# Optimization experiments

Measured on AMD Instinct MI355X. Metric: run time of the kernel, lower is better.

The kernel has to match this reference:

```python
import jax, jax.numpy as jnp
import numpy as np

D_MODEL = 768
D_STATE = 64
HEADDIM = 64
CHUNK = 64
EXPAND = 2
D_CONV = 4
D_INNER = EXPAND * D_MODEL          # 1536
NHEADS = D_INNER // HEADDIM         # 24
CONV_CH = D_INNER + 2 * D_STATE     # 1664
D_IN_PROJ = 2 * D_INNER + 2 * D_STATE + NHEADS  # 3224
EPS = 1e-5


def segsum(x):
    # x: (..., T) -> (..., T, T); entry [i, j] = sum_{k=j+1..i} x[k] for i>=j, -inf above diag
    T = x.shape[-1]
    cs = jnp.cumsum(x, axis=-1)
    seg = cs[..., :, None] - cs[..., None, :]
    mask = jnp.tril(jnp.ones((T, T), dtype=bool))
    return jnp.where(mask, seg, -jnp.inf)


def ssd(x, A, B, C, chunk):
    # x: (b, L, h, p), A: (b, L, h), B/C: (b, L, n)
    b, L, h, p = x.shape
    nc = L // chunk
    x = x.reshape(b, nc, chunk, h, p)
    A = A.reshape(b, nc, chunk, h).transpose(0, 3, 1, 2)   # (b, h, nc, l)
    B = B.reshape(b, nc, chunk, -1)
    C = C.reshape(b, nc, chunk, -1)
    A_cs = jnp.cumsum(A, axis=-1)                          # (b, h, nc, l)
    Lm = jnp.exp(segsum(A))                                # (b, h, nc, l, s)
    # intra-chunk (diagonal) term
    Y_diag = jnp.einsum('bcln,bcsn,bhcls,bcshp->bclhp', C, B, Lm, x)
    # per-chunk states
    decay_states = jnp.exp(A_cs[..., -1:] - A_cs)          # (b, h, nc, l)
    states = jnp.einsum('bcln,bhcl,bclhp->bchpn', B, decay_states, x)
    states = jnp.concatenate([jnp.zeros_like(states[:, :1]), states], axis=1)
    # inter-chunk recurrence via segsum over chunk totals
    chunk_sums = jnp.pad(A_cs[..., -1], ((0, 0), (0, 0), (1, 0)))
    decay_chunk = jnp.exp(segsum(chunk_sums))              # (b, h, nc+1, nc+1)
    new_states = jnp.einsum('bhzc,bchpn->bzhpn', decay_chunk, states)
    states = new_states[:, :-1]                            # (b, nc, h, p, n)
    Y_off = jnp.einsum('bcln,bchpn,bhcl->bclhp', C, states, jnp.exp(A_cs))
    return (Y_diag + Y_off).reshape(b, L, h, p)


def setup_inputs() -> dict:
    key = jax.random.key(0)
    ks = jax.random.split(key, 6)
    b, L = 2, 4096
    u = jax.random.normal(ks[0], (b, L, D_MODEL), dtype=jnp.float32)
    W_in = jax.random.normal(ks[1], (D_IN_PROJ, D_MODEL), dtype=jnp.float32) * (D_MODEL ** -0.5)
    conv_w = jax.random.normal(ks[2], (CONV_CH, 1, D_CONV), dtype=jnp.float32) * 0.3
    conv_b = jnp.zeros((CONV_CH,), dtype=jnp.float32)
    dt_bias = jnp.zeros((NHEADS,), dtype=jnp.float32)
    A_log = jax.random.normal(ks[3], (NHEADS,), dtype=jnp.float32) * 0.1
    D = jnp.ones((NHEADS,), dtype=jnp.float32)
    norm_w = jnp.ones((D_INNER,), dtype=jnp.float32)
    W_out = jax.random.normal(ks[4], (D_MODEL, D_INNER), dtype=jnp.float32) * (D_INNER ** -0.5)
    return {'u': u, 'W_in': W_in, 'conv_w': conv_w, 'conv_b': conv_b,
            'dt_bias': dt_bias, 'A_log': A_log, 'D': D, 'norm_w': norm_w, 'W_out': W_out}


def reference(u, W_in, conv_w, conv_b, dt_bias, A_log, D, norm_w, W_out):
    b, L, _ = u.shape
    zxbcdt = u @ W_in.T                                    # (b, L, d_in_proj)
    z = zxbcdt[..., :D_INNER]
    xBC = zxbcdt[..., D_INNER:D_INNER + CONV_CH]
    dt = jax.nn.softplus(zxbcdt[..., -NHEADS:] + dt_bias)  # (b, L, h)
    # causal depthwise conv (left pad d_conv-1, matches torch pad+slice)
    xBC = jax.lax.conv_general_dilated(
        xBC.transpose(0, 2, 1), conv_w, (1,), [(D_CONV - 1, 0)],
        dimension_numbers=('NCH', 'OIH', 'NCH'), feature_group_count=CONV_CH)
    xBC = jax.nn.silu(xBC.transpose(0, 2, 1) + conv_b)
    x = xBC[..., :D_INNER].reshape(b, L, NHEADS, HEADDIM)
    Bm = xBC[..., D_INNER:D_INNER + D_STATE]
    Cm = xBC[..., -D_STATE:]
    A = -jnp.exp(A_log)                                    # (h,)
    y = ssd(x * dt[..., None], A * dt, Bm, Cm, CHUNK)
    y = y + x * D[None, None, :, None]
    y = y.reshape(b, L, D_INNER)
    # gated RMSNorm
    y = y * jax.nn.silu(z)
    y = y * jax.lax.rsqrt(jnp.mean(y * y, axis=-1, keepdims=True) + EPS) * norm_w
    return y @ W_out.T
```

## Files before the change

### kernel.cpp

```cpp
#include <hip/hip_runtime.h>

typedef __attribute__((ext_vector_type(4))) float f4;
typedef __attribute__((ext_vector_type(8))) short bfx8;
typedef __attribute__((ext_vector_type(4))) float f32x4;
typedef __attribute__((ext_vector_type(4))) unsigned int u32x4;
typedef __attribute__((ext_vector_type(4))) unsigned short u16x4;
typedef __attribute__((ext_vector_type(8))) unsigned short u16x8;
typedef unsigned short ushort_t;

#define DM 768
#define DINNER 1536
#define NH 24
#define XBCW 1664
#define DINPROJ 3224
#define NPAD1 3328
#define NCHUNK 64
#define BROWS 8192
#define PADB 72

__device__ inline ushort_t f2bf(float f) {
    unsigned u = __builtin_bit_cast(unsigned, f);
    unsigned r = (u + 0x7FFF + ((u >> 16) & 1)) >> 16;
    return (ushort_t)r;
}
__device__ inline float bf2f(ushort_t u) {
    return __builtin_bit_cast(float, (unsigned)u << 16);
}
__device__ inline void gl16(const void* g, void* l) {
    __builtin_amdgcn_global_load_lds((const __attribute__((address_space(1))) void*)g,
                                     (__attribute__((address_space(3))) void*)l, 16, 0, 0);
}

__global__ __launch_bounds__(256) void fill_kernel(float* out, int n, float v) {
    int i = blockIdx.x * 256 + threadIdx.x;
    if (i < n) out[i] = v;
}

__global__ __launch_bounds__(256) void cvt_kernel(const float* __restrict__ in,
                                                  ushort_t* __restrict__ outp, long n4) {
    long i = (long)blockIdx.x * 256 + threadIdx.x;
    if (i >= n4) return;
    f4 v = *(const f4*)&in[i * 4];
    u16x4 o;
    o[0] = f2bf(v[0]); o[1] = f2bf(v[1]); o[2] = f2bf(v[2]); o[3] = f2bf(v[3]);
    *(u16x4*)&outp[i * 4] = o;
}

__global__ __launch_bounds__(256) void cvt_pad_kernel(const float* __restrict__ in,
                                                      ushort_t* __restrict__ outp) {
    long q = (long)blockIdx.x * 256 + threadIdx.x;
    if (q >= (long)NPAD1 * 192) return;
    int row = (int)(q / 192);
    int cq = (int)(q % 192);
    u16x4 o = {0, 0, 0, 0};
    if (row < DINPROJ) {
        f4 v = *(const f4*)&in[(long)row * DM + cq * 4];
        o[0] = f2bf(v[0]); o[1] = f2bf(v[1]); o[2] = f2bf(v[2]); o[3] = f2bf(v[3]);
    }
    *(u16x4*)&outp[q * 4] = o;
}

template <int EPI>
__global__ __launch_bounds__(256) void gemm_bt(const ushort_t* __restrict__ A,
                                               const ushort_t* __restrict__ B,
                                               float* __restrict__ C,
                                               int K, int ldc,
                                               ushort_t* __restrict__ zbf,
                                               float* __restrict__ xbcraw,
                                               float* __restrict__ dtbT,
                                               const float* __restrict__ dt_bias) {
    __shared__ __align__(16) ushort_t As[2][128 * 32];
    __shared__ __align__(16) ushort_t Bs[2][128 * 32];
    int tid = threadIdx.x;
    int lane = tid & 63;
    int w = tid >> 6;
    int wr = w >> 1, wc = w & 1;
    int m0 = blockIdx.y * 128;
    int n0 = blockIdx.x * 128;
    int r16 = lane & 15, kg = lane >> 4;

    int row0 = tid >> 2, cof0 = (tid & 3) * 8;
    const ushort_t* a0 = &A[(long)(m0 + row0) * K + cof0];
    const ushort_t* a1 = &A[(long)(m0 + row0 + 64) * K + cof0];
    const ushort_t* b0 = &B[(long)(n0 + row0) * K + cof0];
    const ushort_t* b1 = &B[(long)(n0 + row0 + 64) * K + cof0];
    char* asb[2] = {(char*)&As[0][0] + w * 1024, (char*)&As[1][0] + w * 1024};
    char* bsb[2] = {(char*)&Bs[0][0] + w * 1024, (char*)&Bs[1][0] + w * 1024};

    f32x4 acc[4][4] = {};

    gl16(a0, asb[0]); gl16(a1, asb[0] + 4096);
    gl16(b0, bsb[0]); gl16(b1, bsb[0] + 4096);
    asm volatile("s_waitcnt vmcnt(0)" ::: "memory");
    __builtin_amdgcn_s_barrier();

    int nk = K >> 5;
    for (int t = 0; t < nk; ++t) {
        int cur = t & 1;
        if (t + 1 < nk) {
            int k1 = (t + 1) << 5;
            gl16(a0 + k1, asb[cur ^ 1]); gl16(a1 + k1, asb[cur ^ 1] + 4096);
            gl16(b0 + k1, bsb[cur ^ 1]); gl16(b1 + k1, bsb[cur ^ 1] + 4096);
        }
        const ushort_t* Asc = &As[cur][0];
        const ushort_t* Bsc = &Bs[cur][0];
        bfx8 af[4], bfr[4];
#pragma unroll
        for (int i = 0; i < 4; ++i) {
            af[i] = *(const bfx8*)&Asc[(wr * 64 + i * 16 + r16) * 32 + kg * 8];
            bfr[i] = *(const bfx8*)&Bsc[(wc * 64 + i * 16 + r16) * 32 + kg * 8];
        }
#pragma unroll
        for (int i = 0; i < 4; ++i)
#pragma unroll
            for (int j = 0; j < 4; ++j)
                acc[i][j] = __builtin_amdgcn_mfma_f32_16x16x32_bf16(af[i], bfr[j], acc[i][j], 0, 0, 0);
        asm volatile("s_waitcnt vmcnt(0) lgkmcnt(0)" ::: "memory");
        __builtin_amdgcn_sched_barrier(0);
        __builtin_amdgcn_s_barrier();
    }

#pragma unroll
    for (int i = 0; i < 4; ++i) {
        int rowb = m0 + wr * 64 + i * 16 + kg * 4;
#pragma unroll
        for (int j = 0; j < 4; ++j) {
            int col = n0 + wc * 64 + j * 16 + r16;
            if (EPI == 0) {
#pragma unroll
                for (int q = 0; q < 4; ++q)
                    C[(long)(rowb + q) * ldc + col] = acc[i][j][q];
            } else {
                if (n0 < DINNER) {
#pragma unroll
                    for (int q = 0; q < 4; ++q)
                        zbf[(long)(rowb + q) * DINNER + col] = f2bf(acc[i][j][q]);
                } else if (n0 < 3200) {
#pragma unroll
                    for (int q = 0; q < 4; ++q)
                        xbcraw[(long)(rowb + q) * XBCW + col - DINNER] = acc[i][j][q];
                } else if (col < DINPROJ) {
                    int h = col - 3200;
                    float bias = dt_bias[h];
#pragma unroll
                    for (int q = 0; q < 4; ++q) {
                        float v = acc[i][j][q] + bias;
                        float d = (v > 20.f) ? v : log1pf(__expf(v));
                        dtbT[(long)h * BROWS + rowb + q] = d;
                    }
                }
            }
        }
    }
}

__global__ __launch_bounds__(256) void conv_kernel(const float* __restrict__ xin,
                                                   const float* __restrict__ cw,
                                                   const float* __restrict__ cb,
                                                   ushort_t* __restrict__ xbc) {
    int ch = blockIdx.y * 256 + threadIdx.x;
    int row = blockIdx.x;
    if (ch >= XBCW) return;
    int b = row >> 12;
    int l = row & 4095;
    float acc = cb[ch];
#pragma unroll
    for (int k = 0; k < 4; ++k) {
        int ll = l - 3 + k;
        if (ll >= 0)
            acc += cw[ch * 4 + k] * xin[(long)(b * 4096 + ll) * XBCW + ch];
    }
    float s = acc / (1.f + __expf(-acc));
    xbc[(long)row * XBCW + ch] = f2bf(s);
}

__global__ __launch_bounds__(256) void acs_kernel(const float* __restrict__ dtbT,
                                                  const float* __restrict__ A_log,
                                                  float* __restrict__ acs,
                                                  float* __restrict__ Tsum) {
    int bh = blockIdx.x;
    int b = bh / NH, h = bh % NH;
    int t = threadIdx.x;
    int lane = t & 63;
    float A = -__expf(A_log[h]);
    const float* dp = &dtbT[(long)h * BROWS + b * 4096];
#pragma unroll
    for (int it = 0; it < 16; ++it) {
        int c = (t >> 6) + 4 * it;
        float v = A * dp[c * 64 + lane];
#pragma unroll
        for (int off = 1; off < 64; off <<= 1) {
            float u = __shfl_up(v, off, 64);
            if (lane >= off) v += u;
        }
        acs[((long)bh * NCHUNK + c) * 64 + lane] = v;
        if (lane == 63) Tsum[bh * NCHUNK + c] = v;
    }
}

__global__ __launch_bounds__(256) void states_kernel(const ushort_t* __restrict__ xbc,
                                                     const float* __restrict__ dtbT,
                                                     const float* __restrict__ acs,
                                                     const float* __restrict__ Tsum,
                                                     ushort_t* __restrict__ states) {
    int h = blockIdx.x, c = blockIdx.y, b = blockIdx.z;
    __shared__ __align__(16) ushort_t Wt[64 * PADB];
    __shared__ __align__(16) ushort_t Bt[64 * PADB];
    int t = threadIdx.x;
    long rowg0 = (long)b * 4096 + c * 64;
    long acsb = ((long)(b * NH + h) * NCHUNK + c) * 64;
    float T = Tsum[(b * NH + h) * NCHUNK + c];
#pragma unroll
    for (int i = 0; i < 2; ++i) {
        int q = t + 256 * i;
        int l = q >> 3, sg = q & 7;
        const ushort_t* rp = &xbc[(rowg0 + l) * (long)XBCW];
        float dec = dtbT[(long)h * BROWS + rowg0 + l] * __expf(T - acs[acsb + l]);
        u16x8 xv = *(const u16x8*)&rp[h * 64 + sg * 8];
        u16x8 bv = *(const u16x8*)&rp[DINNER + sg * 8];
#pragma unroll
        for (int jj = 0; jj < 8; ++jj) {
            Wt[(sg * 8 + jj) * PADB + l] = f2bf(bf2f(xv[jj]) * dec);
            Bt[(sg * 8 + jj) * PADB + l] = bv[jj];
        }
    }
    __syncthreads();
    int w = t >> 6, lane = t & 63;
    int r16 = lane & 15, kg = lane >> 4;
    bfx8 aw[2];
#pragma unroll
    for (int kk = 0; kk < 2; ++kk)
        aw[kk] = *(const bfx8*)&Wt[(w * 16 + r16) * PADB + kk * 32 + kg * 8];
    f32x4 acc[4] = {};
#pragma unroll
    for (int j = 0; j < 4; ++j)
#pragma unroll
        for (int kk = 0; kk < 2; ++kk) {
            bfx8 bb = *(const bfx8*)&Bt[(j * 16 + r16) * PADB + kk * 32 + kg * 8];
            acc[j] = __builtin_amdgcn_mfma_f32_16x16x32_bf16(aw[kk], bb, acc[j], 0, 0, 0);
        }
    __syncthreads();
#pragma unroll
    for (int j = 0; j < 4; ++j)
#pragma unroll
        for (int q = 0; q < 4; ++q)
            Wt[(w * 16 + kg * 4 + q) * PADB + j * 16 + r16] = f2bf(acc[j][q]);
    __syncthreads();
    long ob = ((long)(b * NH + h) * NCHUNK + c) * 4096;
#pragma unroll
    for (int i = 0; i < 2; ++i) {
        int q = t + 256 * i;
        int p = q >> 3, sg = q & 7;
        *(u16x8*)&states[ob + p * 64 + sg * 8] = *(const u16x8*)&Wt[p * PADB + sg * 8];
    }
}

__global__ __launch_bounds__(256) void scan_kernel(const float* __restrict__ Tsum,
                                                   ushort_t* __restrict__ states) {
    int e = blockIdx.x * 256 + threadIdx.x;
    int h = blockIdx.y, b = blockIdx.z;
    long base = ((long)(b * NH + h)) * NCHUNK * 4096 + e;
    const float* Tp = &Tsum[(b * NH + h) * NCHUNK];
    float acc = 0.f;
    for (int c = 0; c < NCHUNK; ++c) {
        float cur = bf2f(states[base + (long)c * 4096]);
        states[base + (long)c * 4096] = f2bf(acc);
        acc = __expf(Tp[c]) * acc + cur;
    }
}

__global__ __launch_bounds__(256) void yfull_kernel(const ushort_t* __restrict__ xbc,
                                                    const float* __restrict__ dtbT,
                                                    const float* __restrict__ acs,
                                                    const ushort_t* __restrict__ sprev,
                                                    ushort_t* __restrict__ ybuf) {
    int h = blockIdx.x, c = blockIdx.y, b = blockIdx.z;
    __shared__ __align__(16) ushort_t Cb[64 * PADB];
    __shared__ __align__(16) ushort_t Bb[64 * PADB];
    __shared__ __align__(16) ushort_t Xt[64 * PADB];
    __shared__ __align__(16) ushort_t Sp[64 * PADB];
    __shared__ __align__(16) ushort_t Sm[64 * PADB];
    __shared__ float sAcs[64], sE[64];
    int t = threadIdx.x;
    long rowg0 = (long)b * 4096 + c * 64;
    long acsb = ((long)(b * NH + h) * NCHUNK + c) * 64;
    long spb = ((long)(b * NH + h) * NCHUNK + c) * 4096;
    if (t < 64) {
        float a = acs[acsb + t];
        sAcs[t] = a;
        sE[t] = __expf(a);
    }
#pragma unroll
    for (int i = 0; i < 2; ++i) {
        int q = t + 256 * i;
        int l = q >> 3, sg = q & 7;
        const ushort_t* rp = &xbc[(rowg0 + l) * (long)XBCW];
        *(u16x8*)&Cb[l * PADB + sg * 8] = *(const u16x8*)&rp[1600 + sg * 8];
        *(u16x8*)&Bb[l * PADB + sg * 8] = *(const u16x8*)&rp[DINNER + sg * 8];
        float dtv = dtbT[(long)h * BROWS + rowg0 + l];
        u16x8 xv = *(const u16x8*)&rp[h * 64 + sg * 8];
#pragma unroll
        for (int jj = 0; jj < 8; ++jj)
            Xt[(sg * 8 + jj) * PADB + l] = f2bf(bf2f(xv[jj]) * dtv);
        *(u16x8*)&Sp[l * PADB + sg * 8] = *(const u16x8*)&sprev[spb + l * 64 + sg * 8];
    }
    __syncthreads();
    int w = t >> 6, lane = t & 63;
    int r16 = lane & 15, kg = lane >> 4;
    bfx8 ac[2];
#pragma unroll
    for (int kk = 0; kk < 2; ++kk)
        ac[kk] = *(const bfx8*)&Cb[(w * 16 + r16) * PADB + kk * 32 + kg * 8];
    f32x4 s_acc[4] = {};
#pragma unroll
    for (int j = 0; j < 4; ++j)
#pragma unroll
        for (int kk = 0; kk < 2; ++kk) {
            bfx8 bb = *(const bfx8*)&Bb[(j * 16 + r16) * PADB + kk * 32 + kg * 8];
            s_acc[j] = __builtin_amdgcn_mfma_f32_16x16x32_bf16(ac[kk], bb, s_acc[j], 0, 0, 0);
        }
#pragma unroll
    for (int j = 0; j < 4; ++j)
#pragma unroll
        for (int q = 0; q < 4; ++q) {
            int l = w * 16 + kg * 4 + q;
            int s = j * 16 + r16;
            float v = s_acc[j][q];
            v = (s <= l) ? v * __expf(sAcs[l] - sAcs[s]) : 0.f;
            Sm[l * PADB + s] = f2bf(v);
        }
    __syncthreads();
    bfx8 as[2];
#pragma unroll
    for (int kk = 0; kk < 2; ++kk)
        as[kk] = *(const bfx8*)&Sm[(w * 16 + r16) * PADB + kk * 32 + kg * 8];
    f32x4 d_acc[4] = {}, o_acc[4] = {};
#pragma unroll
    for (int j = 0; j < 4; ++j)
#pragma unroll
        for (int kk = 0; kk < 2; ++kk) {
            bfx8 xb = *(const bfx8*)&Xt[(j * 16 + r16) * PADB + kk * 32 + kg * 8];
            d_acc[j] = __builtin_amdgcn_mfma_f32_16x16x32_bf16(as[kk], xb, d_acc[j], 0, 0, 0);
            bfx8 sb = *(const bfx8*)&Sp[(j * 16 + r16) * PADB + kk * 32 + kg * 8];
            o_acc[j] = __builtin_amdgcn_mfma_f32_16x16x32_bf16(ac[kk], sb, o_acc[j], 0, 0, 0);
        }
#pragma unroll
    for (int j = 0; j < 4; ++j)
#pragma unroll
        for (int q = 0; q < 4; ++q) {
            int l = w * 16 + kg * 4 + q;
            int p = j * 16 + r16;
            Bb[l * PADB + p] = f2bf(d_acc[j][q] + sE[l] * o_acc[j][q]);
        }
    __syncthreads();
#pragma unroll
    for (int i = 0; i < 2; ++i) {
        int q = t + 256 * i;
        int l = q >> 3, sg = q & 7;
        *(u16x8*)&ybuf[(rowg0 + l) * (long)DINNER + h * 64 + sg * 8] =
            *(const u16x8*)&Bb[l * PADB + sg * 8];
    }
}

__global__ __launch_bounds__(256) void norm_kernel(const ushort_t* __restrict__ ybuf,
                                                   const ushort_t* __restrict__ xbc,
                                                   const ushort_t* __restrict__ zbf,
                                                   const float* __restrict__ Dp,
                                                   const float* __restrict__ normw,
                                                   ushort_t* __restrict__ ybf) {
    int row = blockIdx.x;
    int t = threadIdx.x;
    float g[6];
    float ss = 0.f;
#pragma unroll
    for (int i = 0; i < 6; ++i) {
        int j = t + 256 * i;
        int h = j >> 6;
        float x = bf2f(xbc[(long)row * XBCW + j]);
        float yy = bf2f(ybuf[(long)row * DINNER + j]) + x * Dp[h];
        float z = bf2f(zbf[(long)row * DINNER + j]);
        float gz = z / (1.f + __expf(-z));
        float v = yy * gz;
        g[i] = v;
        ss += v * v;
    }
#pragma unroll
    for (int o = 32; o > 0; o >>= 1) ss += __shfl_xor(ss, o, 64);
    __shared__ float wsum[4];
    __shared__ float sscale;
    int w = t >> 6;
    if ((t & 63) == 0) wsum[w] = ss;
    __syncthreads();
    if (t == 0) {
        float tot = wsum[0] + wsum[1] + wsum[2] + wsum[3];
        sscale = rsqrtf(tot / (float)DINNER + 1e-5f);
    }
    __syncthreads();
    float sc = sscale;
#pragma unroll
    for (int i = 0; i < 6; ++i) {
        int j = t + 256 * i;
        ybf[(long)row * DINNER + j] = f2bf(g[i] * sc * normw[j]);
    }
}

extern "C" void kernel_launch(void* const* d_in, const int* in_sizes, int n_in,
                              void* d_out, int out_size, void* d_ws, size_t ws_size,
                              hipStream_t stream) {
    const float* u = (const float*)d_in[0];
    const float* W_in = (const float*)d_in[1];
    const float* conv_w = (const float*)d_in[2];
    const float* conv_b = (const float*)d_in[3];
    const float* dt_bias = (const float*)d_in[4];
    const float* A_log = (const float*)d_in[5];
    const float* Dp = (const float*)d_in[6];
    const float* norm_w = (const float*)d_in[7];
    const float* W_out = (const float*)d_in[8];
    float* out = (float*)d_out;

    char* ws = (char*)d_ws;
    size_t off = 0;
    auto alloc = [&](size_t bytes) {
        void* p = ws + off;
        off += (bytes + 255) & ~(size_t)255;
        return p;
    };
    ushort_t* zbf = (ushort_t*)alloc((size_t)BROWS * DINNER * 2);
    float* xbcraw = (float*)alloc((size_t)BROWS * XBCW * 4);
    ushort_t* xbc = (ushort_t*)alloc((size_t)BROWS * XBCW * 2);
    float* dtbT = (float*)alloc((size_t)NH * BROWS * 4);
    float* acs = (float*)alloc((size_t)2 * NH * NCHUNK * 64 * 4);
    float* Tsum = (float*)alloc((size_t)2 * NH * NCHUNK * 4);
    ushort_t* states = (ushort_t*)alloc((size_t)2 * NH * NCHUNK * 4096 * 2);
    ushort_t* ybuf = (ushort_t*)alloc((size_t)BROWS * DINNER * 2);
    ushort_t* ybf = (ushort_t*)xbcraw;
    ushort_t* ubf = ybuf;
    ushort_t* winbf = states;
    ushort_t* woutbf = states;

    if (off > ws_size) {
        fill_kernel<<<(out_size + 255) / 256, 256, 0, stream>>>(out, out_size, 12345.0f);
        return;
    }

    cvt_kernel<<<(BROWS * DM / 4 + 255) / 256, 256, 0, stream>>>(u, ubf, (long)BROWS * DM / 4);
    cvt_pad_kernel<<<((long)NPAD1 * 192 + 255) / 256, 256, 0, stream>>>(W_in, winbf);

    gemm_bt<1><<<dim3(26, 64), 256, 0, stream>>>(ubf, winbf, nullptr, DM, 0,
                                                 zbf, xbcraw, dtbT, dt_bias);

    conv_kernel<<<dim3(BROWS, 7), 256, 0, stream>>>(xbcraw, conv_w, conv_b, xbc);

    acs_kernel<<<2 * NH, 256, 0, stream>>>(dtbT, A_log, acs, Tsum);
    states_kernel<<<dim3(NH, NCHUNK, 2), 256, 0, stream>>>(xbc, dtbT, acs, Tsum, states);
    scan_kernel<<<dim3(16, NH, 2), 256, 0, stream>>>(Tsum, states);
    yfull_kernel<<<dim3(NH, NCHUNK, 2), 256, 0, stream>>>(xbc, dtbT, acs, states, ybuf);

    norm_kernel<<<BROWS, 256, 0, stream>>>(ybuf, xbc, zbf, Dp, norm_w, ybf);

    cvt_kernel<<<(DM * DINNER / 4 + 255) / 256, 256, 0, stream>>>(W_out, woutbf, (long)DM * DINNER / 4);
    gemm_bt<0><<<dim3(6, 64), 256, 0, stream>>>(ybf, woutbf, out, DINNER, DM,
                                                nullptr, nullptr, nullptr, nullptr);
}
```

Before: 280.2 us.

## Triple-buffer GEMM LDS pipeline and store pre-conv xBC as bf16

The shared bf16 GEMM moves from a double-buffered LDS loop to a three-stage ring. Tiles are prefetched two iterations ahead, and each iteration waits with a partial vmcnt and a single barrier before compute, so global loads overlap more MFMA work. Separately, the raw xBC projection output is written as bf16 instead of fp32, halving the bytes written by the in-projection and read by the conv kernel. This adds LDS usage (48KB per block), which may lower occupancy, and rounds the pre-convolution values to bf16.

Result: no change. 278.7 us (-0.5%).

```diff
diff --git a/kernel.cpp b/kernel.cpp
--- a/kernel.cpp
+++ b/kernel.cpp
@@ -66,11 +66,11 @@
                                                float* __restrict__ C,
                                                int K, int ldc,
                                                ushort_t* __restrict__ zbf,
-                                               float* __restrict__ xbcraw,
+                                               ushort_t* __restrict__ xbcbf,
                                                float* __restrict__ dtbT,
                                                const float* __restrict__ dt_bias) {
-    __shared__ __align__(16) ushort_t As[2][128 * 32];
-    __shared__ __align__(16) ushort_t Bs[2][128 * 32];
+    __shared__ __align__(16) ushort_t As[3][128 * 32];
+    __shared__ __align__(16) ushort_t Bs[3][128 * 32];
     int tid = threadIdx.x;
     int lane = tid & 63;
     int w = tid >> 6;
@@ -84,26 +84,34 @@
     const ushort_t* a1 = &A[(long)(m0 + row0 + 64) * K + cof0];
     const ushort_t* b0 = &B[(long)(n0 + row0) * K + cof0];
     const ushort_t* b1 = &B[(long)(n0 + row0 + 64) * K + cof0];
-    char* asb[2] = {(char*)&As[0][0] + w * 1024, (char*)&As[1][0] + w * 1024};
-    char* bsb[2] = {(char*)&Bs[0][0] + w * 1024, (char*)&Bs[1][0] + w * 1024};
+    char* asb[3] = {(char*)&As[0][0] + w * 1024, (char*)&As[1][0] + w * 1024,
+                    (char*)&As[2][0] + w * 1024};
+    char* bsb[3] = {(char*)&Bs[0][0] + w * 1024, (char*)&Bs[1][0] + w * 1024,
+                    (char*)&Bs[2][0] + w * 1024};
 
     f32x4 acc[4][4] = {};
-
-    gl16(a0, asb[0]); gl16(a1, asb[0] + 4096);
-    gl16(b0, bsb[0]); gl16(b1, bsb[0] + 4096);
-    asm volatile("s_waitcnt vmcnt(0)" ::: "memory");
-    __builtin_amdgcn_s_barrier();
-
     int nk = K >> 5;
+
+    auto issue = [&](int t) {
+        int k = t << 5;
+        int bi = t % 3;
+        gl16(a0 + k, asb[bi]); gl16(a1 + k, asb[bi] + 4096);
+        gl16(b0 + k, bsb[bi]); gl16(b1 + k, bsb[bi] + 4096);
+    };
+    issue(0);
+    issue(1);
+
     for (int t = 0; t < nk; ++t) {
-        int cur = t & 1;
         if (t + 1 < nk) {
-            int k1 = (t + 1) << 5;
-            gl16(a0 + k1, asb[cur ^ 1]); gl16(a1 + k1, asb[cur ^ 1] + 4096);
-            gl16(b0 + k1, bsb[cur ^ 1]); gl16(b1 + k1, bsb[cur ^ 1] + 4096);
-        }
-        const ushort_t* Asc = &As[cur][0];
-        const ushort_t* Bsc = &Bs[cur][0];
+            asm volatile("s_waitcnt vmcnt(4)" ::: "memory");
+        } else {
+            asm volatile("s_waitcnt vmcnt(0)" ::: "memory");
+        }
+        __builtin_amdgcn_s_barrier();
+        __builtin_amdgcn_sched_barrier(0);
+        if (t + 2 < nk) issue(t + 2);
+        const ushort_t* Asc = &As[t % 3][0];
+        const ushort_t* Bsc = &Bs[t % 3][0];
         bfx8 af[4], bfr[4];
 #pragma unroll
         for (int i = 0; i < 4; ++i) {
@@ -115,9 +123,6 @@
 #pragma unroll
             for (int j = 0; j < 4; ++j)
                 acc[i][j] = __builtin_amdgcn_mfma_f32_16x16x32_bf16(af[i], bfr[j], acc[i][j], 0, 0, 0);
-        asm volatile("s_waitcnt vmcnt(0) lgkmcnt(0)" ::: "memory");
-        __builtin_amdgcn_sched_barrier(0);
-        __builtin_amdgcn_s_barrier();
     }
 
 #pragma unroll
@@ -138,7 +143,7 @@
                 } else if (n0 < 3200) {
 #pragma unroll
                     for (int q = 0; q < 4; ++q)
-                        xbcraw[(long)(rowb + q) * XBCW + col - DINNER] = acc[i][j][q];
+                        xbcbf[(long)(rowb + q) * XBCW + col - DINNER] = f2bf(acc[i][j][q]);
                 } else if (col < DINPROJ) {
                     int h = col - 3200;
                     float bias = dt_bias[h];
@@ -154,7 +159,7 @@
     }
 }
 
-__global__ __launch_bounds__(256) void conv_kernel(const float* __restrict__ xin,
+__global__ __launch_bounds__(256) void conv_kernel(const ushort_t* __restrict__ xin,
                                                    const float* __restrict__ cw,
                                                    const float* __restrict__ cb,
                                                    ushort_t* __restrict__ xbc) {
@@ -168,7 +173,7 @@
     for (int k = 0; k < 4; ++k) {
         int ll = l - 3 + k;
         if (ll >= 0)
-            acc += cw[ch * 4 + k] * xin[(long)(b * 4096 + ll) * XBCW + ch];
+            acc += cw[ch * 4 + k] * bf2f(xin[(long)(b * 4096 + ll) * XBCW + ch]);
     }
     float s = acc / (1.f + __expf(-acc));
     xbc[(long)row * XBCW + ch] = f2bf(s);
@@ -426,14 +431,14 @@
         return p;
     };
     ushort_t* zbf = (ushort_t*)alloc((size_t)BROWS * DINNER * 2);
-    float* xbcraw = (float*)alloc((size_t)BROWS * XBCW * 4);
+    ushort_t* xbcrawbf = (ushort_t*)alloc((size_t)BROWS * XBCW * 2);
     ushort_t* xbc = (ushort_t*)alloc((size_t)BROWS * XBCW * 2);
     float* dtbT = (float*)alloc((size_t)NH * BROWS * 4);
     float* acs = (float*)alloc((size_t)2 * NH * NCHUNK * 64 * 4);
     float* Tsum = (float*)alloc((size_t)2 * NH * NCHUNK * 4);
     ushort_t* states = (ushort_t*)alloc((size_t)2 * NH * NCHUNK * 4096 * 2);
     ushort_t* ybuf = (ushort_t*)alloc((size_t)BROWS * DINNER * 2);
-    ushort_t* ybf = (ushort_t*)xbcraw;
+    ushort_t* ybf = xbcrawbf;
     ushort_t* ubf = ybuf;
     ushort_t* winbf = states;
     ushort_t* woutbf = states;
@@ -447,9 +452,9 @@
     cvt_pad_kernel<<<((long)NPAD1 * 192 + 255) / 256, 256, 0, stream>>>(W_in, winbf);
 
     gemm_bt<1><<<dim3(26, 64), 256, 0, stream>>>(ubf, winbf, nullptr, DM, 0,
-                                                 zbf, xbcraw, dtbT, dt_bias);
-
-    conv_kernel<<<dim3(BROWS, 7), 256, 0, stream>>>(xbcraw, conv_w, conv_b, xbc);
+                                                 zbf, xbcrawbf, dtbT, dt_bias);
+
+    conv_kernel<<<dim3(BROWS, 7), 256, 0, stream>>>(xbcrawbf, conv_w, conv_b, xbc);
 
     acs_kernel<<<2 * NH, 256, 0, stream>>>(dtbT, A_log, acs, Tsum);
     states_kernel<<<dim3(NH, NCHUNK, 2), 256, 0, stream>>>(xbc, dtbT, acs, Tsum, states);
```
